# Kernel tuning notes

Hardware: AMD Instinct MI355X
Metric: run time of the kernel (lower is better)

## Reference

```python
import jax, jax.numpy as jnp
import numpy as np

N, E, F = 50000, 800000, 64
GIN_F, H1, H2, OUT = 32, 128, 256, 2


def _lin_init(key, fan_in, fan_out):
    return jax.random.normal(key, (fan_in, fan_out), dtype=jnp.float32) / np.float32(np.sqrt(fan_in))


def setup_inputs() -> dict:
    key = jax.random.key(0)
    ks = jax.random.split(key, 24)
    inp = {
        "x": jax.random.normal(ks[0], (N, F), dtype=jnp.float32),
        "edge_index": jax.random.randint(ks[1], (2, E), 0, N, dtype=jnp.int64),
    }
    # GIN: 3 GINConv layers, each MLP = Linear->ReLU->Linear, then output Linear
    dims = [GIN_F, H1, H1]
    k = 2
    for i, din in enumerate(dims):
        inp[f"g{i}_w1"] = _lin_init(ks[k], din, H1); k += 1
        inp[f"g{i}_b1"] = jnp.zeros((H1,), jnp.float32)
        inp[f"g{i}_w2"] = _lin_init(ks[k], H1, H1); k += 1
        inp[f"g{i}_b2"] = jnp.zeros((H1,), jnp.float32)
    inp["gout_w"] = _lin_init(ks[k], H1, H1); k += 1
    inp["gout_b"] = jnp.zeros((H1,), jnp.float32)
    # SAGE: 2 SAGEConv layers (mean aggregation)
    sdims = [(F + H1, H2), (H2, OUT)]
    for i, (din, dout) in enumerate(sdims):
        inp[f"s{i}_wl"] = _lin_init(ks[k], din, dout); k += 1
        inp[f"s{i}_wr"] = _lin_init(ks[k], din, dout); k += 1
        inp[f"s{i}_b"] = jnp.zeros((dout,), jnp.float32)
    return inp


def _agg_sum(h, src, dst, n):
    # gather messages at src, scatter-add into dst: [N, d]
    return jax.ops.segment_sum(h[src], dst, num_segments=n)


def _forward(x, edge_index, g0_w1, g0_b1, g0_w2, g0_b2, g1_w1, g1_b1, g1_w2, g1_b2,
             g2_w1, g2_b1, g2_w2, g2_b2, gout_w, gout_b,
             s0_wl, s0_wr, s0_b, s1_wl, s1_wr, s1_b):
    src, dst = edge_index[0], edge_index[1]
    n = x.shape[0]
    deg = jax.ops.segment_sum(jnp.ones((src.shape[0],), x.dtype), dst, num_segments=n)
    inv_deg = (1.0 / jnp.maximum(deg, 1.0))[:, None]  # [N,1]

    # GIN branch on selected features (indices 0..31)
    h = x[:, :GIN_F]
    for w1, b1, w2, b2 in ((g0_w1, g0_b1, g0_w2, g0_b2),
                           (g1_w1, g1_b1, g1_w2, g1_b2),
                           (g2_w1, g2_b1, g2_w2, g2_b2)):
        m = h + _agg_sum(h, src, dst, n)        # (1+eps)*x + sum_neigh, eps=0
        h = jax.nn.relu(jax.nn.relu(m @ w1 + b1) @ w2 + b2)
    gin_out = h @ gout_w + gout_b               # [N, H1]

    # concat raw features with GIN embedding
    h = jnp.concatenate([x, gin_out], axis=1)   # [N, F+H1]

    # SAGE branch (mean aggregation)
    mean1 = _agg_sum(h, src, dst, n) * inv_deg
    h = jax.nn.relu(h @ s0_wl + mean1 @ s0_wr + s0_b)
    mean2 = _agg_sum(h, src, dst, n) * inv_deg
    out = h @ s1_wl + mean2 @ s1_wr + s1_b      # [N, OUT]
    return out


def reference(x, edge_index, g0_w1, g0_b1, g0_w2, g0_b2, g1_w1, g1_b1, g1_w2, g1_b2,
              g2_w1, g2_b1, g2_w2, g2_b2, gout_w, gout_b,
              s0_wl, s0_wr, s0_b, s1_wl, s1_wr, s1_b):
    return _forward(x, edge_index, g0_w1, g0_b1, g0_w2, g0_b2, g1_w1, g1_b1, g1_w2, g1_b2,
                    g2_w1, g2_b1, g2_w2, g2_b2, gout_w, gout_b,
                    s0_wl, s0_wr, s0_b, s1_wl, s1_wr, s1_b)
```

## Files before the change

kernel.cpp:

```cpp
#include <hip/hip_runtime.h>


typedef unsigned short ushort_t;
typedef __bf16 bf16x8 __attribute__((ext_vector_type(8)));
typedef float f32x4 __attribute__((ext_vector_type(4)));

__device__ __forceinline__ float b2f(unsigned int u16) {
    union { unsigned int i; float f; } v;
    v.i = u16 << 16;
    return v.f;
}
__device__ __forceinline__ unsigned short f2b(float f) {
    union { float f; unsigned int i; } v;
    v.f = f;
    unsigned int x = v.i;
    unsigned int r = (x + 0x7fffu + ((x >> 16) & 1u)) >> 16;
    return (unsigned short)r;
}

__global__ void detect_kernel(const int* __restrict__ ei, int ncheck, int* flag) {
    int t = blockIdx.x * blockDim.x + threadIdx.x;
    if (t < ncheck) {
        if (ei[2 * t + 1] != 0) atomicAnd(flag, 0);
    }
}

__global__ void convert_kernel(const int* __restrict__ ei, int E, const int* __restrict__ flag,
                               int* __restrict__ src, int* __restrict__ dst) {
    int e = blockIdx.x * blockDim.x + threadIdx.x;
    if (e >= E) return;
    if (*flag) {
        src[e] = ei[2 * (size_t)e];
        dst[e] = ei[2 * ((size_t)E + e)];
    } else {
        src[e] = ei[e];
        dst[e] = ei[(size_t)E + e];
    }
}

__global__ void deg_kernel(const int* __restrict__ dst, int E, int* __restrict__ deg) {
    int e = blockIdx.x * blockDim.x + threadIdx.x;
    if (e < E) atomicAdd(&deg[dst[e]], 1);
}

__global__ __launch_bounds__(256) void scanA_kernel(const int* __restrict__ deg, int n,
                                                    int* __restrict__ rowptr,
                                                    int* __restrict__ blocksum) {
    __shared__ int sh[256];
    int b = blockIdx.x, tid = threadIdx.x;
    int base = b * 2048 + tid * 8;
    int v[8];
#pragma unroll
    for (int e = 0; e < 8; ++e) {
        int i = base + e;
        v[e] = (i < n) ? deg[i] : 0;
    }
    int t = 0;
#pragma unroll
    for (int e = 0; e < 8; ++e) { int x = v[e]; v[e] = t; t += x; }
    sh[tid] = t;
    __syncthreads();
    for (int off = 1; off < 256; off <<= 1) {
        int val = (tid >= off) ? sh[tid - off] : 0;
        __syncthreads();
        sh[tid] += val;
        __syncthreads();
    }
    int excl = sh[tid] - t;
#pragma unroll
    for (int e = 0; e < 8; ++e) {
        int i = base + e;
        if (i < n) rowptr[i] = excl + v[e];
    }
    if (tid == 255) blocksum[b] = sh[255];
}

__global__ __launch_bounds__(256) void scanB_kernel(const int* __restrict__ blocksum, int nb,
                                                    int* __restrict__ blockoff,
                                                    int* __restrict__ rowptr, int n) {
    __shared__ int sh[256];
    int tid = threadIdx.x;
    int v = (tid < nb) ? blocksum[tid] : 0;
    sh[tid] = v;
    __syncthreads();
    for (int off = 1; off < 256; off <<= 1) {
        int t = (tid >= off) ? sh[tid - off] : 0;
        __syncthreads();
        sh[tid] += t;
        __syncthreads();
    }
    if (tid < nb) blockoff[tid] = sh[tid] - v;
    if (tid == 255) rowptr[n] = sh[255];
}

__global__ void scanC_kernel(const int* __restrict__ deg, int n, const int* __restrict__ blockoff,
                             int* __restrict__ rowptr, int* __restrict__ cursor,
                             float* __restrict__ invdeg) {
    int i = blockIdx.x * blockDim.x + threadIdx.x;
    if (i >= n) return;
    int r = rowptr[i] + blockoff[i >> 11];
    rowptr[i] = r;
    cursor[i] = r;
    invdeg[i] = 1.0f / fmaxf((float)deg[i], 1.0f);
}

__global__ void scatter_kernel(const int* __restrict__ src, const int* __restrict__ dst, int E,
                               int* __restrict__ cursor, int* __restrict__ col) {
    int e = blockIdx.x * blockDim.x + threadIdx.x;
    if (e < E) {
        int p = atomicAdd(&cursor[dst[e]], 1);
        col[p] = src[e];
    }
}

__global__ void xconv_kernel(const float* __restrict__ x, ushort_t* __restrict__ xb, int total16) {
    int idx = blockIdx.x * blockDim.x + threadIdx.x;
    if (idx >= total16) return;
    float4 v = *(const float4*)&x[(size_t)idx * 4];
    ushort4 u;
    u.x = f2b(v.x); u.y = f2b(v.y); u.z = f2b(v.z); u.w = f2b(v.w);
    *(ushort4*)&xb[(size_t)idx * 4] = u;
}

struct WtDesc { const float* src; ushort_t* dst; int lk2; int K; int N; int base; };
struct WtArgs { WtDesc d[11]; int total; };
__global__ void wtconv_kernel(WtArgs a) {
    int idx = blockIdx.x * blockDim.x + threadIdx.x;
    if (idx >= a.total) return;
    int s = 0;
#pragma unroll
    for (int i = 1; i < 11; ++i) if (idx >= a.d[i].base) s = i;
    int local = idx - a.d[s].base;
    int K = a.d[s].K;
    int n = local >> a.d[s].lk2;
    int k = local & (K - 1);
    unsigned off = (unsigned)((n >> 4) * (K >> 5) + (k >> 5)) * 512u
                 + (unsigned)(((n & 15) | (((k >> 3) & 3) << 4)) << 3) + (unsigned)(k & 7);
    a.d[s].dst[off] = f2b(a.d[s].src[(size_t)k * a.d[s].N + n]);
}

template <int VEC>
__device__ __forceinline__ void ldrow(const ushort_t* p, float* t) {
    if constexpr (VEC == 1) {
        t[0] = b2f(p[0]);
    } else if constexpr (VEC == 2) {
        unsigned int v = *(const unsigned int*)p;
        t[0] = b2f(v & 0xffffu); t[1] = b2f(v >> 16);
    } else {
        uint2 v = *(const uint2*)p;
        t[0] = b2f(v.x & 0xffffu); t[1] = b2f(v.x >> 16);
        t[2] = b2f(v.y & 0xffffu); t[3] = b2f(v.y >> 16);
    }
}

template <int VEC, int MODE>
__global__ __launch_bounds__(256) void aggb_kernel(
    const ushort_t* __restrict__ h, int ldh,
    const int* __restrict__ rowptr, const int* __restrict__ col,
    const float* __restrict__ invdeg,
    ushort_t* __restrict__ out, int ldo, int Nn, int lanes) {
    int wid = blockIdx.x * 4 + ((int)threadIdx.x >> 6);
    int lane = (int)threadIdx.x & 63;
    if (wid >= Nn || lane >= lanes) return;

    const ushort_t* hb = h + (size_t)lane * VEC;
    float a[VEC];
#pragma unroll
    for (int v = 0; v < VEC; ++v) a[v] = 0.f;

    int p0 = rowptr[wid], p1 = rowptr[wid + 1];
    int p = p0;
    for (; p + 4 <= p1; p += 4) {
        int j0 = col[p], j1 = col[p + 1], j2 = col[p + 2], j3 = col[p + 3];
        float t0[VEC], t1[VEC], t2[VEC], t3[VEC];
        ldrow<VEC>(hb + (size_t)j0 * ldh, t0);
        ldrow<VEC>(hb + (size_t)j1 * ldh, t1);
        ldrow<VEC>(hb + (size_t)j2 * ldh, t2);
        ldrow<VEC>(hb + (size_t)j3 * ldh, t3);
#pragma unroll
        for (int v = 0; v < VEC; ++v) a[v] += (t0[v] + t1[v]) + (t2[v] + t3[v]);
    }
    for (; p < p1; ++p) {
        float t[VEC];
        ldrow<VEC>(hb + (size_t)col[p] * ldh, t);
#pragma unroll
        for (int v = 0; v < VEC; ++v) a[v] += t[v];
    }

    if constexpr (MODE == 0) {
        float t[VEC];
        ldrow<VEC>(hb + (size_t)wid * ldh, t);
#pragma unroll
        for (int v = 0; v < VEC; ++v) a[v] += t[v];
    } else {
        float s = invdeg[wid];
#pragma unroll
        for (int v = 0; v < VEC; ++v) a[v] *= s;
    }

    ushort_t* op = out + (size_t)wid * ldo + (size_t)lane * VEC;
    if constexpr (VEC == 1) {
        op[0] = f2b(a[0]);
    } else if constexpr (VEC == 2) {
        unsigned int v = (unsigned int)f2b(a[0]) | ((unsigned int)f2b(a[1]) << 16);
        *(unsigned int*)op = v;
    } else {
        uint2 v;
        v.x = (unsigned int)f2b(a[0]) | ((unsigned int)f2b(a[1]) << 16);
        v.y = (unsigned int)f2b(a[2]) | ((unsigned int)f2b(a[3]) << 16);
        *(uint2*)op = v;
    }
}

__global__ __launch_bounds__(256) void aggdual_kernel(
    const ushort_t* __restrict__ xb,
    const int* __restrict__ rowptr, const int* __restrict__ col,
    const float* __restrict__ invdeg,
    ushort_t* __restrict__ out32, ushort_t* __restrict__ out64, int Nn) {
    int wid = blockIdx.x * 4 + ((int)threadIdx.x >> 6);
    int lane = (int)threadIdx.x & 63;
    if (wid >= Nn) return;
    const ushort_t* hb = xb + lane;
    float a = 0.f;
    int p = rowptr[wid], p1 = rowptr[wid + 1];
    for (; p + 4 <= p1; p += 4) {
        float v0 = b2f(hb[(size_t)col[p] * 64]);
        float v1 = b2f(hb[(size_t)col[p + 1] * 64]);
        float v2 = b2f(hb[(size_t)col[p + 2] * 64]);
        float v3 = b2f(hb[(size_t)col[p + 3] * 64]);
        a += (v0 + v1) + (v2 + v3);
    }
    for (; p < p1; ++p) a += b2f(hb[(size_t)col[p] * 64]);
    out64[(size_t)wid * 64 + lane] = f2b(a * invdeg[wid]);
    if (lane < 32) {
        float self = b2f(hb[(size_t)wid * 64]);
        out32[(size_t)wid * 32 + lane] = f2b(a + self);
    }
}

struct GPass { const ushort_t* A; const ushort_t* Wp; int lda; int K; };
struct FArgs {
    GPass p[4]; int np;
    const ushort_t* W2p; const ushort_t* W3p;
    const float* b1; const float* b2; const float* b3;
    int relu1, relu2, relu3;
    int chain;
};

__global__ __launch_bounds__(512) void fgemm_kernel(
    FArgs fa, int M, ushort_t* __restrict__ out, int ldc) {
    __shared__ __align__(16) ushort_t Tlds[4 * 64 * 40];

    int rowbase = blockIdx.x * 64;
    int colbase = blockIdx.y * 128;
    int tid = threadIdx.x;
    int lane = tid & 63, wid = tid >> 6;
    int wr3 = wid & 3, wc2 = wid >> 2;
    int lr = lane & 15, lk = (lane >> 4) * 8, rq = (lane >> 4) * 4;

    f32x4 acc[4];
#pragma unroll
    for (int j = 0; j < 4; ++j) acc[j] = (f32x4){0.f, 0.f, 0.f, 0.f};

    for (int q = 0; q < fa.np; ++q) {
        const ushort_t* A = fa.p[q].A;
        const ushort_t* Wp = fa.p[q].Wp;
        int lda = fa.p[q].lda, K = fa.p[q].K;
        int nch = K >> 5;
        for (int u = tid; u < 256 * nch; u += 512) {
            int c = u >> 8, r = (u >> 2) & 63, seg = u & 3;
            int gr = rowbase + r;
            uint4 va = make_uint4(0u, 0u, 0u, 0u);
            if (gr < M) va = *(const uint4*)&A[(size_t)gr * lda + c * 32 + seg * 8];
            *(uint4*)&Tlds[c * 2560 + r * 40 + seg * 8] = va;
        }
        __syncthreads();
        int cg0 = (colbase >> 4) + wc2 * 4;
        for (int c = 0; c < nch; ++c) {
            bf16x8 af = *(const bf16x8*)&Tlds[c * 2560 + (wr3 * 16 + lr) * 40 + lk];
            bf16x8 bfr[4];
#pragma unroll
            for (int j = 0; j < 4; ++j)
                bfr[j] = *(const bf16x8*)&Wp[((size_t)(cg0 + j) * nch + c) * 512 + lane * 8];
#pragma unroll
            for (int j = 0; j < 4; ++j)
                acc[j] = __builtin_amdgcn_mfma_f32_16x16x32_bf16(af, bfr[j], acc[j], 0, 0, 0);
        }
        __syncthreads();
    }

    for (int g = 2; g <= fa.chain; ++g) {
        const float* bprev = (g == 2) ? fa.b1 : fa.b2;
        int reluprev = (g == 2) ? fa.relu1 : fa.relu2;
        const ushort_t* Wp = (g == 2) ? fa.W2p : fa.W3p;
#pragma unroll
        for (int j = 0; j < 4; ++j) {
            int colj = wc2 * 64 + j * 16 + lr;
            float bv = bprev[colj];
#pragma unroll
            for (int t = 0; t < 4; ++t) {
                int row = wr3 * 16 + rq + t;
                float v = acc[j][t] + bv;
                if (reluprev) v = fmaxf(v, 0.f);
                Tlds[(colj >> 5) * 2560 + row * 40 + (colj & 31)] = f2b(v);
            }
            acc[j] = (f32x4){0.f, 0.f, 0.f, 0.f};
        }
        __syncthreads();
        int cg0 = wc2 * 4;
        for (int c = 0; c < 4; ++c) {
            bf16x8 af = *(const bf16x8*)&Tlds[c * 2560 + (wr3 * 16 + lr) * 40 + lk];
            bf16x8 bfr[4];
#pragma unroll
            for (int j = 0; j < 4; ++j)
                bfr[j] = *(const bf16x8*)&Wp[((size_t)(cg0 + j) * 4 + c) * 512 + lane * 8];
#pragma unroll
            for (int j = 0; j < 4; ++j)
                acc[j] = __builtin_amdgcn_mfma_f32_16x16x32_bf16(af, bfr[j], acc[j], 0, 0, 0);
        }
        __syncthreads();
    }

    const float* bf_ = (fa.chain == 1) ? fa.b1 : (fa.chain == 2) ? fa.b2 : fa.b3;
    int reluf = (fa.chain == 1) ? fa.relu1 : (fa.chain == 2) ? fa.relu2 : fa.relu3;
#pragma unroll
    for (int j = 0; j < 4; ++j) {
        int colj = wc2 * 64 + j * 16 + lr;
        float bv = bf_[colbase + colj];
#pragma unroll
        for (int t = 0; t < 4; ++t) {
            int row = wr3 * 16 + rq + t;
            float v = acc[j][t] + bv;
            if (reluf) v = fmaxf(v, 0.f);
            Tlds[row * 128 + colj] = f2b(v);
        }
    }
    __syncthreads();
    for (int u = tid; u < 1024; u += 512) {
        int row = u >> 4, seg = u & 15;
        int gr = rowbase + row;
        if (gr < M)
            *(uint4*)&out[(size_t)gr * ldc + colbase + seg * 8] =
                *(const uint4*)&Tlds[row * 128 + seg * 8];
    }
}

__global__ void zproj_kernel(const ushort_t* __restrict__ s0,
                             const float* __restrict__ wl, const float* __restrict__ wr,
                             float2* __restrict__ zl, float2* __restrict__ z, int M) {
    int wave = threadIdx.x >> 6;
    int lane = threadIdx.x & 63;
    int i = blockIdx.x * 4 + wave;
    if (i >= M) return;
    float l0 = 0.f, l1 = 0.f, r0 = 0.f, r1 = 0.f;
    for (int k = lane; k < 256; k += 64) {
        float hv = b2f(s0[(size_t)i * 256 + k]);
        float2 wlv = *(const float2*)&wl[2 * k];
        float2 wrv = *(const float2*)&wr[2 * k];
        l0 += hv * wlv.x; l1 += hv * wlv.y;
        r0 += hv * wrv.x; r1 += hv * wrv.y;
    }
#pragma unroll
    for (int off = 32; off > 0; off >>= 1) {
        l0 += __shfl_down(l0, off);
        l1 += __shfl_down(l1, off);
        r0 += __shfl_down(r0, off);
        r1 += __shfl_down(r1, off);
    }
    if (lane == 0) {
        zl[i] = make_float2(l0, l1);
        z[i] = make_float2(r0, r1);
    }
}

__global__ void aggz_kernel(const float2* __restrict__ z, const float2* __restrict__ zl,
                            const int* __restrict__ rowptr, const int* __restrict__ col,
                            const float* __restrict__ invdeg, const float* __restrict__ b,
                            float* __restrict__ out, int Nn) {
    int i = blockIdx.x * blockDim.x + threadIdx.x;
    if (i >= Nn) return;
    float s0 = 0.f, s1 = 0.f;
    int p = rowptr[i], p1 = rowptr[i + 1];
    for (; p + 4 <= p1; p += 4) {
        float2 a = z[col[p]], c = z[col[p + 1]], d = z[col[p + 2]], e = z[col[p + 3]];
        s0 += (a.x + c.x) + (d.x + e.x);
        s1 += (a.y + c.y) + (d.y + e.y);
    }
    for (; p < p1; ++p) {
        float2 a = z[col[p]];
        s0 += a.x; s1 += a.y;
    }
    float inv = invdeg[i];
    float2 l = zl[i];
    out[(size_t)i * 2 + 0] = l.x + inv * s0 + b[0];
    out[(size_t)i * 2 + 1] = l.y + inv * s1 + b[1];
}

extern "C" void kernel_launch(void* const* d_in, const int* in_sizes, int n_in,
                              void* d_out, int out_size, void* d_ws, size_t ws_size,
                              hipStream_t stream) {
    const float* x      = (const float*)d_in[0];
    const int*   ei     = (const int*)d_in[1];
    const float* g_w1[3] = {(const float*)d_in[2], (const float*)d_in[6],  (const float*)d_in[10]};
    const float* g_b1[3] = {(const float*)d_in[3], (const float*)d_in[7],  (const float*)d_in[11]};
    const float* g_w2[3] = {(const float*)d_in[4], (const float*)d_in[8],  (const float*)d_in[12]};
    const float* g_b2[3] = {(const float*)d_in[5], (const float*)d_in[9],  (const float*)d_in[13]};
    const float* gout_w = (const float*)d_in[14];
    const float* gout_b = (const float*)d_in[15];
    const float* s0_wl  = (const float*)d_in[16];
    const float* s0_wr  = (const float*)d_in[17];
    const float* s0_b   = (const float*)d_in[18];
    const float* s1_wl  = (const float*)d_in[19];
    const float* s1_wr  = (const float*)d_in[20];
    const float* s1_b   = (const float*)d_in[21];
    float* out = (float*)d_out;

    const int N = in_sizes[0] / 64;
    const int E = in_sizes[1] / 2;

    char* ws = (char*)d_ws;
    size_t o = 0;
    auto take = [&](size_t bytes) -> char* {
        char* p = ws + o;
        o = (o + bytes + 255) & ~(size_t)255;
        return p;
    };
    ushort_t* xb     = (ushort_t*)take((size_t)N * 64 * 2);
    ushort_t* bA     = (ushort_t*)take((size_t)N * 128 * 2);
    ushort_t* bB     = (ushort_t*)take((size_t)N * 128 * 2);
    ushort_t* bC     = (ushort_t*)take((size_t)N * 128 * 2);
    ushort_t* ginb   = (ushort_t*)take((size_t)N * 128 * 2);
    ushort_t* aggxb  = (ushort_t*)take((size_t)N * 64 * 2);
    ushort_t* agggb  = (ushort_t*)take((size_t)N * 128 * 2);
    ushort_t* s0b    = (ushort_t*)take((size_t)N * 256 * 2);
    float2*   zlb    = (float2*)take((size_t)N * 2 * 4);
    float2*   zb     = (float2*)take((size_t)N * 2 * 4);
    ushort_t* w1t0 = (ushort_t*)take(128 * 32 * 2);
    ushort_t* w2t0 = (ushort_t*)take(128 * 128 * 2);
    ushort_t* w1t1 = (ushort_t*)take(128 * 128 * 2);
    ushort_t* w2t1 = (ushort_t*)take(128 * 128 * 2);
    ushort_t* w1t2 = (ushort_t*)take(128 * 128 * 2);
    ushort_t* w2t2 = (ushort_t*)take(128 * 128 * 2);
    ushort_t* goutt = (ushort_t*)take(128 * 128 * 2);
    ushort_t* wltop = (ushort_t*)take(256 * 64 * 2);
    ushort_t* wlbot = (ushort_t*)take(256 * 128 * 2);
    ushort_t* wrtop = (ushort_t*)take(256 * 64 * 2);
    ushort_t* wrbot = (ushort_t*)take(256 * 128 * 2);
    int*   srcI   = (int*)take((size_t)E * 4);
    int*   dstI   = (int*)take((size_t)E * 4);
    int*   colI   = (int*)take((size_t)E * 4);
    int*   rowptr = (int*)take((size_t)(N + 1) * 4);
    int*   cursor = (int*)take((size_t)N * 4);
    int*   deg    = (int*)take((size_t)N * 4);
    float* invdeg = (float*)take((size_t)N * 4);
    int*   blocksum = (int*)take(256 * 4);
    int*   blockoff = (int*)take(256 * 4);
    int*   flag   = (int*)take(4);

    hipMemsetAsync(deg, 0, (size_t)N * 4, stream);
    hipMemsetAsync(flag, 1, 4, stream);

    const int TB = 256;
    const int nb = (N + 2047) / 2048;

    detect_kernel<<<4, TB, 0, stream>>>(ei, 1024, flag);
    convert_kernel<<<(E + TB - 1) / TB, TB, 0, stream>>>(ei, E, flag, srcI, dstI);
    deg_kernel<<<(E + TB - 1) / TB, TB, 0, stream>>>(dstI, E, deg);
    scanA_kernel<<<nb, 256, 0, stream>>>(deg, N, rowptr, blocksum);
    scanB_kernel<<<1, 256, 0, stream>>>(blocksum, nb, blockoff, rowptr, N);
    scanC_kernel<<<(N + TB - 1) / TB, TB, 0, stream>>>(deg, N, blockoff, rowptr, cursor, invdeg);
    scatter_kernel<<<(E + TB - 1) / TB, TB, 0, stream>>>(srcI, dstI, E, cursor, colI);

    WtArgs wa;
    const float* wsrc[11] = {g_w1[0], g_w2[0], g_w1[1], g_w2[1], g_w1[2], g_w2[2], gout_w,
                             s0_wl, s0_wl + 64 * 256, s0_wr, s0_wr + 64 * 256};
    ushort_t* wdst[11]    = {w1t0, w2t0, w1t1, w2t1, w1t2, w2t2, goutt,
                             wltop, wlbot, wrtop, wrbot};
    int wk[11]  = {32, 128, 128, 128, 128, 128, 128, 64, 128, 64, 128};
    int wl2[11] = {5, 7, 7, 7, 7, 7, 7, 6, 7, 6, 7};
    int wn[11]  = {128, 128, 128, 128, 128, 128, 128, 256, 256, 256, 256};
    int base = 0;
    for (int i = 0; i < 11; ++i) {
        wa.d[i].src = wsrc[i]; wa.d[i].dst = wdst[i];
        wa.d[i].lk2 = wl2[i]; wa.d[i].K = wk[i]; wa.d[i].N = wn[i]; wa.d[i].base = base;
        base += wk[i] * wn[i];
    }
    wa.total = base;
    wtconv_kernel<<<(base + TB - 1) / TB, TB, 0, stream>>>(wa);

    xconv_kernel<<<((N * 16) + TB - 1) / TB, TB, 0, stream>>>(x, xb, N * 16);

    const int AGG_GRID = (N + 3) / 4;
    const int GX = (N + 63) / 64;

    aggdual_kernel<<<AGG_GRID, 256, 0, stream>>>(xb, rowptr, colI, invdeg, bB, aggxb, N);

    {
        FArgs fa = {};
        fa.p[0] = {bB, w1t0, 32, 32};
        fa.np = 1;
        fa.W2p = w2t0;
        fa.b1 = g_b1[0]; fa.b2 = g_b2[0];
        fa.relu1 = 1; fa.relu2 = 1;
        fa.chain = 2;
        fgemm_kernel<<<dim3(GX, 1), 512, 0, stream>>>(fa, N, bA, 128);
    }

    aggb_kernel<2, 0><<<AGG_GRID, 256, 0, stream>>>(bA, 128, rowptr, colI, invdeg, bB, 128, N, 64);
    {
        FArgs fa = {};
        fa.p[0] = {bB, w1t1, 128, 128};
        fa.np = 1;
        fa.W2p = w2t1;
        fa.b1 = g_b1[1]; fa.b2 = g_b2[1];
        fa.relu1 = 1; fa.relu2 = 1;
        fa.chain = 2;
        fgemm_kernel<<<dim3(GX, 1), 512, 0, stream>>>(fa, N, bC, 128);
    }

    aggb_kernel<2, 0><<<AGG_GRID, 256, 0, stream>>>(bC, 128, rowptr, colI, invdeg, bB, 128, N, 64);
    {
        FArgs fa = {};
        fa.p[0] = {bB, w1t2, 128, 128};
        fa.np = 1;
        fa.W2p = w2t2; fa.W3p = goutt;
        fa.b1 = g_b1[2]; fa.b2 = g_b2[2]; fa.b3 = gout_b;
        fa.relu1 = 1; fa.relu2 = 1; fa.relu3 = 0;
        fa.chain = 3;
        fgemm_kernel<<<dim3(GX, 1), 512, 0, stream>>>(fa, N, ginb, 128);
    }

    aggb_kernel<2, 1><<<AGG_GRID, 256, 0, stream>>>(ginb, 128, rowptr, colI, invdeg, agggb, 128, N, 64);

    {
        FArgs fa = {};
        fa.p[0] = {xb, wltop, 64, 64};
        fa.p[1] = {ginb, wlbot, 128, 128};
        fa.p[2] = {aggxb, wrtop, 64, 64};
        fa.p[3] = {agggb, wrbot, 128, 128};
        fa.np = 4;
        fa.b1 = s0_b;
        fa.relu1 = 1;
        fa.chain = 1;
        fgemm_kernel<<<dim3(GX, 2), 512, 0, stream>>>(fa, N, s0b, 256);
    }

    zproj_kernel<<<(N + 3) / 4, 256, 0, stream>>>(s0b, s1_wl, s1_wr, zlb, zb, N);
    aggz_kernel<<<(N + TB - 1) / TB, TB, 0, stream>>>(zb, zlb, rowptr, colI, invdeg, s1_b, out, N);
}
```

Before: 381.5 us.

## Fold GIN output linear into SAGE weights and bucket-sort CSR build

Precomputes gout_w·s0_wl and gout_w·s0_wr (plus the bias terms) so the third GIN GEMM chain no longer runs the output projection, and the mean-aggregated bias is applied through a per-row nonzero-degree mask. It also replaces the convert/scatter CSR construction with a two-pass bucketed binning (block-local LDS sort by destination bucket, then per-bucket placement), removing the src/dst intermediate arrays and scattered global atomics. The costs are a small weight-fold kernel and one more launch, plus a change in bf16 rounding from folding weights. The 16-bit src packing assumes fewer than 65536 nodes.

```diff
diff --git a/kernel.cpp b/kernel.cpp
--- a/kernel.cpp
+++ b/kernel.cpp
@@ -25,22 +25,12 @@
     }
 }
 
-__global__ void convert_kernel(const int* __restrict__ ei, int E, const int* __restrict__ flag,
-                               int* __restrict__ src, int* __restrict__ dst) {
+__global__ void deg_kernel(const int* __restrict__ ei, int E, const int* __restrict__ flag,
+                           int* __restrict__ deg) {
     int e = blockIdx.x * blockDim.x + threadIdx.x;
     if (e >= E) return;
-    if (*flag) {
-        src[e] = ei[2 * (size_t)e];
-        dst[e] = ei[2 * ((size_t)E + e)];
-    } else {
-        src[e] = ei[e];
-        dst[e] = ei[(size_t)E + e];
-    }
-}
-
-__global__ void deg_kernel(const int* __restrict__ dst, int E, int* __restrict__ deg) {
-    int e = blockIdx.x * blockDim.x + threadIdx.x;
-    if (e < E) atomicAdd(&deg[dst[e]], 1);
+    int d = (*flag) ? ei[2 * ((size_t)E + e)] : ei[(size_t)E + e];
+    atomicAdd(&deg[d], 1);
 }
 
 __global__ __launch_bounds__(256) void scanA_kernel(const int* __restrict__ deg, int n,
@@ -94,22 +84,94 @@
 }
 
 __global__ void scanC_kernel(const int* __restrict__ deg, int n, const int* __restrict__ blockoff,
-                             int* __restrict__ rowptr, int* __restrict__ cursor,
-                             float* __restrict__ invdeg) {
+                             int* __restrict__ rowptr, float* __restrict__ invdeg,
+                             float* __restrict__ mask) {
     int i = blockIdx.x * blockDim.x + threadIdx.x;
     if (i >= n) return;
-    int r = rowptr[i] + blockoff[i >> 11];
-    rowptr[i] = r;
-    cursor[i] = r;
-    invdeg[i] = 1.0f / fmaxf((float)deg[i], 1.0f);
-}
-
-__global__ void scatter_kernel(const int* __restrict__ src, const int* __restrict__ dst, int E,
-                               int* __restrict__ cursor, int* __restrict__ col) {
-    int e = blockIdx.x * blockDim.x + threadIdx.x;
-    if (e < E) {
-        int p = atomicAdd(&cursor[dst[e]], 1);
-        col[p] = src[e];
+    rowptr[i] = rowptr[i] + blockoff[i >> 11];
+    int d = deg[i];
+    invdeg[i] = 1.0f / fmaxf((float)d, 1.0f);
+    mask[i] = (d > 0) ? 1.0f : 0.0f;
+}
+
+__global__ void bucketinit_kernel(const int* __restrict__ rowptr, int Nn, int nbkt,
+                                  int* __restrict__ bucket_cursor) {
+    int b = blockIdx.x * blockDim.x + threadIdx.x;
+    if (b < nbkt) bucket_cursor[b] = rowptr[min(b << 8, Nn)];
+}
+
+__global__ __launch_bounds__(256) void binA_kernel(
+    const int* __restrict__ ei, int E, const int* __restrict__ flag,
+    int* __restrict__ bucket_cursor, unsigned* __restrict__ stage) {
+    __shared__ unsigned sPair[4096];
+    __shared__ int cnt[256], off[256];
+    int tid = threadIdx.x;
+    cnt[tid] = 0;
+    __syncthreads();
+    int base = blockIdx.x * 4096;
+    bool i64 = (*flag) != 0;
+    unsigned u[16];
+    int bk[16];
+#pragma unroll
+    for (int k = 0; k < 16; ++k) {
+        int e = base + tid + k * 256;
+        if (e < E) {
+            int s_, d_;
+            if (i64) { s_ = ei[2 * (size_t)e]; d_ = ei[2 * ((size_t)E + e)]; }
+            else     { s_ = ei[e];             d_ = ei[(size_t)E + e]; }
+            bk[k] = d_ >> 8;
+            u[k] = (unsigned)s_ | ((unsigned)(d_ & 255) << 16);
+            atomicAdd(&cnt[bk[k]], 1);
+        } else bk[k] = -1;
+    }
+    __syncthreads();
+    int c = cnt[tid];
+    off[tid] = c;
+    __syncthreads();
+    for (int o = 1; o < 256; o <<= 1) {
+        int v = (tid >= o) ? off[tid - o] : 0;
+        __syncthreads();
+        off[tid] += v;
+        __syncthreads();
+    }
+    int incl = off[tid];
+    __syncthreads();
+    off[tid] = incl - c;
+    __syncthreads();
+#pragma unroll
+    for (int k = 0; k < 16; ++k) {
+        if (bk[k] >= 0) {
+            int p = atomicAdd(&off[bk[k]], 1);
+            sPair[p] = u[k];
+        }
+    }
+    __syncthreads();
+    int lane = tid & 63, w = tid >> 6;
+    for (int b = w; b < 256; b += 4) {
+        int cb = cnt[b];
+        if (cb == 0) continue;
+        int st = off[b] - cb;
+        int gp;
+        if (lane == 0) gp = atomicAdd(&bucket_cursor[b], cb);
+        gp = __shfl(gp, 0);
+        for (int kk = lane; kk < cb; kk += 64) stage[gp + kk] = sPair[st + kk];
+    }
+}
+
+__global__ __launch_bounds__(256) void binB_kernel(
+    const unsigned* __restrict__ stage, const int* __restrict__ rowptr,
+    int Nn, int* __restrict__ col) {
+    __shared__ int curs[256];
+    int b = blockIdx.x, tid = threadIdx.x;
+    int n0 = b << 8;
+    if (n0 + tid < Nn) curs[tid] = rowptr[n0 + tid];
+    __syncthreads();
+    int s = rowptr[n0];
+    int e = rowptr[min(n0 + 256, Nn)];
+    for (int i = s + tid; i < e; i += 256) {
+        unsigned u = stage[i];
+        int p = atomicAdd(&curs[(u >> 16) & 255], 1);
+        col[p] = (int)(u & 0xffffu);
     }
 }
 
@@ -122,14 +184,44 @@
     *(ushort4*)&xb[(size_t)idx * 4] = u;
 }
 
+__global__ void foldw_kernel(const float* __restrict__ gw, const float* __restrict__ gb,
+                             const float* __restrict__ s0wl, const float* __restrict__ s0wr,
+                             const float* __restrict__ s0bias,
+                             float* __restrict__ Fl, float* __restrict__ Fr,
+                             float* __restrict__ bias2, float* __restrict__ cvec) {
+    int idx = blockIdx.x * blockDim.x + threadIdx.x;
+    if (idx >= 128 * 256) return;
+    int k = idx >> 8, n = idx & 255;
+    const float* wl = s0wl + 64 * 256;
+    const float* wr = s0wr + 64 * 256;
+    float al = 0.f, ar = 0.f;
+    for (int j = 0; j < 128; ++j) {
+        float g = gw[k * 128 + j];
+        al += g * wl[j * 256 + n];
+        ar += g * wr[j * 256 + n];
+    }
+    Fl[k * 256 + n] = al;
+    Fr[k * 256 + n] = ar;
+    if (k == 0) {
+        float bl = 0.f, br = 0.f;
+        for (int j = 0; j < 128; ++j) {
+            float g = gb[j];
+            bl += g * wl[j * 256 + n];
+            br += g * wr[j * 256 + n];
+        }
+        bias2[n] = s0bias[n] + bl;
+        cvec[n] = br;
+    }
+}
+
 struct WtDesc { const float* src; ushort_t* dst; int lk2; int K; int N; int base; };
-struct WtArgs { WtDesc d[11]; int total; };
+struct WtArgs { WtDesc d[10]; int total; };
 __global__ void wtconv_kernel(WtArgs a) {
     int idx = blockIdx.x * blockDim.x + threadIdx.x;
     if (idx >= a.total) return;
     int s = 0;
 #pragma unroll
-    for (int i = 1; i < 11; ++i) if (idx >= a.d[i].base) s = i;
+    for (int i = 1; i < 10; ++i) if (idx >= a.d[i].base) s = i;
     int local = idx - a.d[s].base;
     int K = a.d[s].K;
     int n = local >> a.d[s].lk2;
@@ -245,6 +337,7 @@
     const float* b1; const float* b2; const float* b3;
     int relu1, relu2, relu3;
     int chain;
+    const float* rowmask; const float* cvec;
 };
 
 __global__ __launch_bounds__(512) void fgemm_kernel(
@@ -323,14 +416,21 @@
 
     const float* bf_ = (fa.chain == 1) ? fa.b1 : (fa.chain == 2) ? fa.b2 : fa.b3;
     int reluf = (fa.chain == 1) ? fa.relu1 : (fa.chain == 2) ? fa.relu2 : fa.relu3;
+    float rm[4];
+#pragma unroll
+    for (int t = 0; t < 4; ++t) {
+        int gr = rowbase + wr3 * 16 + rq + t;
+        rm[t] = (fa.cvec && gr < M) ? fa.rowmask[gr] : 0.f;
+    }
 #pragma unroll
     for (int j = 0; j < 4; ++j) {
         int colj = wc2 * 64 + j * 16 + lr;
         float bv = bf_[colbase + colj];
+        float cv = fa.cvec ? fa.cvec[colbase + colj] : 0.f;
 #pragma unroll
         for (int t = 0; t < 4; ++t) {
             int row = wr3 * 16 + rq + t;
-            float v = acc[j][t] + bv;
+            float v = acc[j][t] + bv + rm[t] * cv;
             if (reluf) v = fmaxf(v, 0.f);
             Tlds[row * 128 + colj] = f2b(v);
         }
@@ -429,32 +529,34 @@
     ushort_t* bA     = (ushort_t*)take((size_t)N * 128 * 2);
     ushort_t* bB     = (ushort_t*)take((size_t)N * 128 * 2);
     ushort_t* bC     = (ushort_t*)take((size_t)N * 128 * 2);
-    ushort_t* ginb   = (ushort_t*)take((size_t)N * 128 * 2);
     ushort_t* aggxb  = (ushort_t*)take((size_t)N * 64 * 2);
     ushort_t* agggb  = (ushort_t*)take((size_t)N * 128 * 2);
     ushort_t* s0b    = (ushort_t*)take((size_t)N * 256 * 2);
     float2*   zlb    = (float2*)take((size_t)N * 2 * 4);
     float2*   zb     = (float2*)take((size_t)N * 2 * 4);
+    float* Flbuf = (float*)take(128 * 256 * 4);
+    float* Frbuf = (float*)take(128 * 256 * 4);
+    float* bias2 = (float*)take(256 * 4);
+    float* cvecb = (float*)take(256 * 4);
     ushort_t* w1t0 = (ushort_t*)take(128 * 32 * 2);
     ushort_t* w2t0 = (ushort_t*)take(128 * 128 * 2);
     ushort_t* w1t1 = (ushort_t*)take(128 * 128 * 2);
     ushort_t* w2t1 = (ushort_t*)take(128 * 128 * 2);
     ushort_t* w1t2 = (ushort_t*)take(128 * 128 * 2);
     ushort_t* w2t2 = (ushort_t*)take(128 * 128 * 2);
-    ushort_t* goutt = (ushort_t*)take(128 * 128 * 2);
     ushort_t* wltop = (ushort_t*)take(256 * 64 * 2);
-    ushort_t* wlbot = (ushort_t*)take(256 * 128 * 2);
+    ushort_t* wglp  = (ushort_t*)take(256 * 128 * 2);
     ushort_t* wrtop = (ushort_t*)take(256 * 64 * 2);
-    ushort_t* wrbot = (ushort_t*)take(256 * 128 * 2);
-    int*   srcI   = (int*)take((size_t)E * 4);
-    int*   dstI   = (int*)take((size_t)E * 4);
+    ushort_t* wgrp  = (ushort_t*)take(256 * 128 * 2);
+    unsigned* stage  = (unsigned*)take((size_t)E * 4);
     int*   colI   = (int*)take((size_t)E * 4);
     int*   rowptr = (int*)take((size_t)(N + 1) * 4);
-    int*   cursor = (int*)take((size_t)N * 4);
     int*   deg    = (int*)take((size_t)N * 4);
     float* invdeg = (float*)take((size_t)N * 4);
+    float* maskb  = (float*)take((size_t)N * 4);
     int*   blocksum = (int*)take(256 * 4);
     int*   blockoff = (int*)take(256 * 4);
+    int*   bucket_cursor = (int*)take(512 * 4);
     int*   flag   = (int*)take(4);
 
     hipMemsetAsync(deg, 0, (size_t)N * 4, stream);
@@ -462,25 +564,29 @@
 
     const int TB = 256;
     const int nb = (N + 2047) / 2048;
+    const int NBKT = (N + 255) >> 8;
 
     detect_kernel<<<4, TB, 0, stream>>>(ei, 1024, flag);
-    convert_kernel<<<(E + TB - 1) / TB, TB, 0, stream>>>(ei, E, flag, srcI, dstI);
-    deg_kernel<<<(E + TB - 1) / TB, TB, 0, stream>>>(dstI, E, deg);
+    deg_kernel<<<(E + TB - 1) / TB, TB, 0, stream>>>(ei, E, flag, deg);
     scanA_kernel<<<nb, 256, 0, stream>>>(deg, N, rowptr, blocksum);
     scanB_kernel<<<1, 256, 0, stream>>>(blocksum, nb, blockoff, rowptr, N);
-    scanC_kernel<<<(N + TB - 1) / TB, TB, 0, stream>>>(deg, N, blockoff, rowptr, cursor, invdeg);
-    scatter_kernel<<<(E + TB - 1) / TB, TB, 0, stream>>>(srcI, dstI, E, cursor, colI);
-
+    scanC_kernel<<<(N + TB - 1) / TB, TB, 0, stream>>>(deg, N, blockoff, rowptr, invdeg, maskb);
+    bucketinit_kernel<<<(NBKT + 255) / 256, 256, 0, stream>>>(rowptr, N, NBKT, bucket_cursor);
+    binA_kernel<<<(E + 4095) / 4096, 256, 0, stream>>>(ei, E, flag, bucket_cursor, stage);
+    binB_kernel<<<NBKT, 256, 0, stream>>>(stage, rowptr, N, colI);
+
+    foldw_kernel<<<128, 256, 0, stream>>>(gout_w, gout_b, s0_wl, s0_wr, s0_b,
+                                          Flbuf, Frbuf, bias2, cvecb);
     WtArgs wa;
-    const float* wsrc[11] = {g_w1[0], g_w2[0], g_w1[1], g_w2[1], g_w1[2], g_w2[2], gout_w,
-                             s0_wl, s0_wl + 64 * 256, s0_wr, s0_wr + 64 * 256};
-    ushort_t* wdst[11]    = {w1t0, w2t0, w1t1, w2t1, w1t2, w2t2, goutt,
-                             wltop, wlbot, wrtop, wrbot};
-    int wk[11]  = {32, 128, 128, 128, 128, 128, 128, 64, 128, 64, 128};
-    int wl2[11] = {5, 7, 7, 7, 7, 7, 7, 6, 7, 6, 7};
-    int wn[11]  = {128, 128, 128, 128, 128, 128, 128, 256, 256, 256, 256};
+    const float* wsrc[10] = {g_w1[0], g_w2[0], g_w1[1], g_w2[1], g_w1[2], g_w2[2],
+                             s0_wl, Flbuf, s0_wr, Frbuf};
+    ushort_t* wdst[10]    = {w1t0, w2t0, w1t1, w2t1, w1t2, w2t2,
+                             wltop, wglp, wrtop, wgrp};
+    int wk[10]  = {32, 128, 128, 128, 128, 128, 64, 128, 64, 128};
+    int wl2[10] = {5, 7, 7, 7, 7, 7, 6, 7, 6, 7};
+    int wn[10]  = {128, 128, 128, 128, 128, 128, 256, 256, 256, 256};
     int base = 0;
-    for (int i = 0; i < 11; ++i) {
+    for (int i = 0; i < 10; ++i) {
         wa.d[i].src = wsrc[i]; wa.d[i].dst = wdst[i];
         wa.d[i].lk2 = wl2[i]; wa.d[i].K = wk[i]; wa.d[i].N = wn[i]; wa.d[i].base = base;
         base += wk[i] * wn[i];
@@ -523,25 +629,26 @@
         FArgs fa = {};
         fa.p[0] = {bB, w1t2, 128, 128};
         fa.np = 1;
-        fa.W2p = w2t2; fa.W3p = goutt;
-        fa.b1 = g_b1[2]; fa.b2 = g_b2[2]; fa.b3 = gout_b;
-        fa.relu1 = 1; fa.relu2 = 1; fa.relu3 = 0;
-        fa.chain = 3;
-        fgemm_kernel<<<dim3(GX, 1), 512, 0, stream>>>(fa, N, ginb, 128);
-    }
-
-    aggb_kernel<2, 1><<<AGG_GRID, 256, 0, stream>>>(ginb, 128, rowptr, colI, invdeg, agggb, 128, N, 64);
+        fa.W2p = w2t2;
+        fa.b1 = g_b1[2]; fa.b2 = g_b2[2];
+        fa.relu1 = 1; fa.relu2 = 1;
+        fa.chain = 2;
+        fgemm_kernel<<<dim3(GX, 1), 512, 0, stream>>>(fa, N, bA, 128);
+    }
+
+    aggb_kernel<2, 1><<<AGG_GRID, 256, 0, stream>>>(bA, 128, rowptr, colI, invdeg, agggb, 128, N, 64);
 
     {
         FArgs fa = {};
         fa.p[0] = {xb, wltop, 64, 64};
-        fa.p[1] = {ginb, wlbot, 128, 128};
+        fa.p[1] = {bA, wglp, 128, 128};
         fa.p[2] = {aggxb, wrtop, 64, 64};
-        fa.p[3] = {agggb, wrbot, 128, 128};
+        fa.p[3] = {agggb, wgrp, 128, 128};
         fa.np = 4;
-        fa.b1 = s0_b;
+        fa.b1 = bias2;
         fa.relu1 = 1;
         fa.chain = 1;
+        fa.rowmask = maskb; fa.cvec = cvecb;
         fgemm_kernel<<<dim3(GX, 2), 512, 0, stream>>>(fa, N, s0b, 256);
     }
 
```

New measurement: 543.2 us. 1.42x slower.
